# Kernel tuning notes

Hardware: AMD Instinct MI355X
Metric: run time of the kernel (lower is better)

Reference implementation:

```python
import jax, jax.numpy as jnp
import numpy as np

K = 3  # reassembly kernel size (hardcoded in module)
S = 2  # upsample scale (hardcoded)
PAD = K // 2


def _nearest_up2(t):
    # F.interpolate(scale_factor=2, mode='nearest') on NCHW
    return jnp.repeat(jnp.repeat(t, 2, axis=2), 2, axis=3)


def _patches3x3(t):
    # F.unfold(kernel=3, pad=1) -> [B, C, 9, H, W], k = ki*3 + kj (row-major)
    B, C, H, W = t.shape
    tp = jnp.pad(t, ((0, 0), (0, 0), (PAD, PAD), (PAD, PAD)))
    return jnp.stack([tp[:, :, i:i + H, j:j + W] for i in range(K) for j in range(K)], axis=2)


def setup_inputs() -> dict:
    key = jax.random.key(0)
    k1, k2 = jax.random.split(key)
    x = jax.random.normal(k1, (2, 256, 128, 128), dtype=jnp.float32)
    W_off = jax.random.normal(k2, (2, 1, 5, 5), dtype=jnp.float32) * 1e-3  # normal_init std=0.001
    b_off = jnp.zeros((2,), dtype=jnp.float32)
    return {"x": x, "W_off": W_off, "b_off": b_off}


def reference(x, W_off, b_off):
    B, C, H, W = x.shape
    H2, W2 = S * H, S * W

    mean = jnp.mean(x, axis=1, keepdims=True)  # [B,1,H,W]

    # offset = tanh(conv5x5(nearest_up2(mean))) / 4 -> [B,2,2H,2W]
    mean_up = _nearest_up2(mean)
    off = jax.lax.conv_general_dilated(mean_up, W_off, (1, 1), ((2, 2), (2, 2)))
    offset = jnp.tanh(off + b_off[None, :, None, None]) / 4.0

    # center buffer: pixel_shuffle of [1,8,1,1]; per 2x2 cell, channel 0 varies with j, channel 1 with i
    cell = jnp.array([[[-0.25, 0.25], [-0.25, 0.25]],
                      [[-0.25, -0.25], [0.25, 0.25]]], dtype=x.dtype)  # [2(ch),2(i),2(j)]
    center = jnp.broadcast_to(cell[:, None, :, None, :], (2, H, 2, W, 2)).reshape(2, H2, W2)

    shift = center[None] + offset  # [B,2,2H,2W]

    # neighbor grid: n0 (fast, width) = [-1,0,1]*3 ; n1 (slow, height) = repeat([-1,0,1],3)
    n0 = jnp.tile(jnp.array([-1.0, 0.0, 1.0], dtype=x.dtype), 3)        # [9]
    n1 = jnp.repeat(jnp.array([-1.0, 0.0, 1.0], dtype=x.dtype), 3)      # [9]
    d2 = (shift[:, 0:1] - n0[None, :, None, None]) ** 2 + \
         (shift[:, 1:2] - n1[None, :, None, None]) ** 2                 # [B,9,2H,2W]
    kernels = 1.0 / (d2 + 0.2)

    # grad gating from 3x3 neighborhood of mean
    pm = _patches3x3(mean)[:, 0]            # [B,9,H,W]
    grad = pm - mean                        # broadcast over k
    grad = 1.0 / (grad ** 2 + 1.0)
    logits = _nearest_up2(grad) * kernels   # [B,9,2H,2W]
    kernels = jax.nn.softmax(logits, axis=1)

    # CARAFE: out[b,c,2h+p,2w+q] = sum_k kernels[b,k,2h+p,2w+q] * patches[b,c,k,h,w]
    patches = _patches3x3(x)                        # [B,C,9,H,W]
    Kr = kernels.reshape(B, K * K, H, S, W, S)      # [B,9,H,2,W,2]
    out = jnp.einsum('bkhpwq,bckhw->bchpwq', Kr, patches).reshape(B, C, H2, W2)
    return out
```

## Files before the change

kernel.cpp:

```cpp
#include <hip/hip_runtime.h>
#include <math.h>

#define B 2
#define C 256
#define H 128
#define W 128
#define H2 256
#define W2 256
#define CPT 8
#define TW 16

__global__ __launch_bounds__(1024) void mean_kernel(const float* __restrict__ x,
                                                    float* __restrict__ mean) {
    int bh = blockIdx.x;
    int b = bh / H, h = bh % H;
    int tid = threadIdx.x;
    int g  = tid >> 5;
    int w4 = tid & 31;

    const float4* xb = (const float4*)x + (size_t)b * C * (H * W / 4)
                       + (size_t)h * (W / 4) + w4;
    const size_t cstride = H * W / 4;

    float4 acc = make_float4(0.f, 0.f, 0.f, 0.f);
    #pragma unroll
    for (int i = 0; i < C / 32; ++i) {
        float4 v = xb[(size_t)(g * (C / 32) + i) * cstride];
        acc.x += v.x; acc.y += v.y; acc.z += v.z; acc.w += v.w;
    }

    __shared__ float4 sm[1024];
    sm[tid] = acc;
    __syncthreads();
    for (int s = 16; s >= 1; s >>= 1) {
        if (g < s) {
            float4 o = sm[tid + s * 32];
            acc.x += o.x; acc.y += o.y; acc.z += o.z; acc.w += o.w;
            sm[tid] = acc;
        }
        __syncthreads();
    }
    if (g == 0) {
        const float inv = 1.0f / C;
        float4 m = make_float4(acc.x * inv, acc.y * inv, acc.z * inv, acc.w * inv);
        ((float4*)mean)[(size_t)bh * (W / 4) + w4] = m;
    }
}

__global__ __launch_bounds__(256) void weights_kernel(const float* __restrict__ mean,
                                                      const float* __restrict__ Woff,
                                                      const float* __restrict__ boff,
                                                      float* __restrict__ Kw) {
    __shared__ float sm[10][12];
    __shared__ float sW[50];
    __shared__ float sb[2];

    int b  = blockIdx.z;
    int x0 = blockIdx.x * TW;
    int y0 = blockIdx.y * TW;
    int h0 = y0 >> 1, w0 = x0 >> 1;
    int tid = threadIdx.x;

    if (tid < 100) {
        int lh = tid / 10, lw = tid % 10;
        int hh = h0 - 1 + lh, ww = w0 - 1 + lw;
        sm[lh][lw] = (hh >= 0 && hh < H && ww >= 0 && ww < W)
                         ? mean[(size_t)b * H * W + hh * W + ww] : 0.f;
    }
    if (tid >= 128 && tid < 178) sW[tid - 128] = Woff[tid - 128];
    if (tid >= 192 && tid < 194) sb[tid - 192] = boff[tid - 192];
    __syncthreads();

    int tx = tid & 15, ty = tid >> 4;
    int y = y0 + ty, x = x0 + tx;

    float off0 = 0.f, off1 = 0.f;
    #pragma unroll
    for (int u = 0; u < 5; ++u) {
        int lh = ((y + u - 2) >> 1) - (h0 - 1);
        #pragma unroll
        for (int v = 0; v < 5; ++v) {
            int lw = ((x + v - 2) >> 1) - (w0 - 1);
            float m = sm[lh][lw];
            off0 += m * sW[u * 5 + v];
            off1 += m * sW[25 + u * 5 + v];
        }
    }
    float s0 = tanhf(off0 + sb[0]) * 0.25f + ((x & 1) ? 0.25f : -0.25f);
    float s1 = tanhf(off1 + sb[1]) * 0.25f + ((y & 1) ? 0.25f : -0.25f);

    int lhc = (ty >> 1) + 1;
    int lwc = (tx >> 1) + 1;
    float mc = sm[lhc][lwc];

    float lg[9];
    float mx = -1e30f;
    #pragma unroll
    for (int k = 0; k < 9; ++k) {
        int di = k / 3 - 1, dj = k % 3 - 1;
        float pm = sm[lhc + di][lwc + dj];
        float g = pm - mc;
        float grad = 1.0f / (g * g + 1.0f);
        float d0 = s0 - (float)dj;
        float d1 = s1 - (float)di;
        float kern = 1.0f / (d0 * d0 + d1 * d1 + 0.2f);
        float l = grad * kern;
        lg[k] = l;
        mx = fmaxf(mx, l);
    }
    float sum = 0.f;
    #pragma unroll
    for (int k = 0; k < 9; ++k) { lg[k] = expf(lg[k] - mx); sum += lg[k]; }
    float inv = 1.0f / sum;

    float* o = Kw + (size_t)b * 9 * (H2 * W2) + (size_t)y * W2 + x;
    #pragma unroll
    for (int k = 0; k < 9; ++k) o[(size_t)k * (H2 * W2)] = lg[k] * inv;
}

__global__ __launch_bounds__(256) void carafe_kernel(const float* __restrict__ x,
                                                     const float* __restrict__ Kw,
                                                     float* __restrict__ out) {
    int idx = blockIdx.x * blockDim.x + threadIdx.x;
    int w  = idx % W;
    int h  = (idx / W) % H;
    int cg = (idx / (W * H)) % (C / CPT);
    int b  = idx / (W * H * (C / CPT));

    int y0 = 2 * h, x0 = 2 * w;
    const float* kb = Kw + (size_t)b * 9 * (H2 * W2);

    float2 wk[2][9];
    #pragma unroll
    for (int k = 0; k < 9; ++k) {
        const float* kp = kb + (size_t)k * (H2 * W2) + (size_t)y0 * W2 + x0;
        wk[0][k] = *(const float2*)kp;
        wk[1][k] = *(const float2*)(kp + W2);
    }

    const float* xb = x   + (size_t)(b * C + cg * CPT) * (H * W);
    float*       ob = out + (size_t)(b * C + cg * CPT) * (H2 * W2);

    int poff[9]; bool pval[9];
    #pragma unroll
    for (int k = 0; k < 9; ++k) {
        int di = k / 3 - 1, dj = k % 3 - 1;
        int hh = h + di, ww = w + dj;
        pval[k] = (hh >= 0) & (hh < H) & (ww >= 0) & (ww < W);
        poff[k] = hh * W + ww;
    }

    #pragma unroll 2
    for (int cc = 0; cc < CPT; ++cc) {
        float p[9];
        #pragma unroll
        for (int k = 0; k < 9; ++k)
            p[k] = pval[k] ? xb[poff[k]] : 0.f;
        #pragma unroll
        for (int pp = 0; pp < 2; ++pp) {
            float2 acc = make_float2(0.f, 0.f);
            #pragma unroll
            for (int k = 0; k < 9; ++k) {
                acc.x += wk[pp][k].x * p[k];
                acc.y += wk[pp][k].y * p[k];
            }
            *(float2*)(ob + (size_t)(y0 + pp) * W2 + x0) = acc;
        }
        xb += H * W;
        ob += H2 * W2;
    }
}

extern "C" void kernel_launch(void* const* d_in, const int* in_sizes, int n_in,
                              void* d_out, int out_size, void* d_ws, size_t ws_size,
                              hipStream_t stream) {
    const float* x    = (const float*)d_in[0];
    const float* Woff = (const float*)d_in[1];
    const float* boff = (const float*)d_in[2];
    float* out = (float*)d_out;

    float* mean = (float*)d_ws;
    float* Kw   = mean + (size_t)B * H * W;

    mean_kernel<<<B * H, 1024, 0, stream>>>(x, mean);

    dim3 wgrid(W2 / TW, H2 / TW, B);
    weights_kernel<<<wgrid, 256, 0, stream>>>(mean, Woff, boff, Kw);

    int mt = B * (C / CPT) * H * W;
    carafe_kernel<<<mt / 256, 256, 0, stream>>>(x, Kw, out);
}
```

Measured before the change: 177.0 us.

## Process two input columns per thread and 16 channels in CARAFE kernel

Result: no change. 175.3 us (-1.0%).

```diff
diff --git a/kernel.cpp b/kernel.cpp
--- a/kernel.cpp
+++ b/kernel.cpp
@@ -7,7 +7,7 @@
 #define W 128
 #define H2 256
 #define W2 256
-#define CPT 8
+#define CPT 16
 #define TW 16
 
 __global__ __launch_bounds__(1024) void mean_kernel(const float* __restrict__ x,
@@ -122,49 +122,61 @@
                                                      const float* __restrict__ Kw,
                                                      float* __restrict__ out) {
     int idx = blockIdx.x * blockDim.x + threadIdx.x;
-    int w  = idx % W;
-    int h  = (idx / W) % H;
-    int cg = (idx / (W * H)) % (C / CPT);
-    int b  = idx / (W * H * (C / CPT));
-
+    int w2 = idx & 63;
+    int h  = (idx >> 6) & (H - 1);
+    int cg = (idx >> 13) & (C / CPT - 1);
+    int b  = idx >> 17;
+
+    int w  = w2 * 2;
     int y0 = 2 * h, x0 = 2 * w;
-    const float* kb = Kw + (size_t)b * 9 * (H2 * W2);
-
-    float2 wk[2][9];
+
+    const float* kb = Kw + (size_t)b * 9 * (H2 * W2) + (size_t)y0 * W2 + x0;
+    float4 wk[2][9];
     #pragma unroll
     for (int k = 0; k < 9; ++k) {
-        const float* kp = kb + (size_t)k * (H2 * W2) + (size_t)y0 * W2 + x0;
-        wk[0][k] = *(const float2*)kp;
-        wk[1][k] = *(const float2*)(kp + W2);
+        wk[0][k] = *(const float4*)(kb + (size_t)k * (H2 * W2));
+        wk[1][k] = *(const float4*)(kb + (size_t)k * (H2 * W2) + W2);
+    }
+
+    int off[3][4]; bool val[3][4];
+    #pragma unroll
+    for (int r = 0; r < 3; ++r) {
+        int hh = h - 1 + r;
+        #pragma unroll
+        for (int c = 0; c < 4; ++c) {
+            int ww = w - 1 + c;
+            val[r][c] = (hh >= 0) & (hh < H) & (ww >= 0) & (ww < W);
+            off[r][c] = hh * W + ww;
+        }
     }
 
     const float* xb = x   + (size_t)(b * C + cg * CPT) * (H * W);
-    float*       ob = out + (size_t)(b * C + cg * CPT) * (H2 * W2);
-
-    int poff[9]; bool pval[9];
-    #pragma unroll
-    for (int k = 0; k < 9; ++k) {
-        int di = k / 3 - 1, dj = k % 3 - 1;
-        int hh = h + di, ww = w + dj;
-        pval[k] = (hh >= 0) & (hh < H) & (ww >= 0) & (ww < W);
-        poff[k] = hh * W + ww;
-    }
+    float*       ob = out + (size_t)(b * C + cg * CPT) * (H2 * W2)
+                          + (size_t)y0 * W2 + x0;
 
     #pragma unroll 2
     for (int cc = 0; cc < CPT; ++cc) {
-        float p[9];
-        #pragma unroll
-        for (int k = 0; k < 9; ++k)
-            p[k] = pval[k] ? xb[poff[k]] : 0.f;
+        float p[3][4];
+        #pragma unroll
+        for (int r = 0; r < 3; ++r)
+            #pragma unroll
+            for (int c = 0; c < 4; ++c)
+                p[r][c] = val[r][c] ? xb[off[r][c]] : 0.f;
+
         #pragma unroll
         for (int pp = 0; pp < 2; ++pp) {
-            float2 acc = make_float2(0.f, 0.f);
+            float4 acc = make_float4(0.f, 0.f, 0.f, 0.f);
             #pragma unroll
             for (int k = 0; k < 9; ++k) {
-                acc.x += wk[pp][k].x * p[k];
-                acc.y += wk[pp][k].y * p[k];
+                int ki = k / 3, kj = k % 3;
+                float a  = p[ki][kj];
+                float bb = p[ki][kj + 1];
+                acc.x += wk[pp][k].x * a;
+                acc.y += wk[pp][k].y * a;
+                acc.z += wk[pp][k].z * bb;
+                acc.w += wk[pp][k].w * bb;
             }
-            *(float2*)(ob + (size_t)(y0 + pp) * W2 + x0) = acc;
+            *(float4*)(ob + (size_t)pp * W2) = acc;
         }
         xb += H * W;
         ob += H2 * W2;
@@ -187,6 +199,6 @@
     dim3 wgrid(W2 / TW, H2 / TW, B);
     weights_kernel<<<wgrid, 256, 0, stream>>>(mean, Woff, boff, Kw);
 
-    int mt = B * (C / CPT) * H * W;
+    int mt = B * (C / CPT) * H * (W / 2);
     carafe_kernel<<<mt / 256, 256, 0, stream>>>(x, Kw, out);
 }
```
